# Kernel tuning notes

Measured on AMD Instinct MI355X. Metric: run time of the kernel, lower is better.

Reference implementation:

```python
import jax, jax.numpy as jnp
import numpy as np

N_GRAPHS = 4
NODES_PER_GRAPH = 8192
N_NODES = N_GRAPHS * NODES_PER_GRAPH
N_EDGES = N_NODES * 16
IN_DIM = 3
HID = 128
K_OUT = 512
MAX_WAVELENGTH = 10000.0


def _glorot(k, shape):
    lim = (6.0 / (shape[0] + shape[1])) ** 0.5
    return jax.random.uniform(k, shape, jnp.float32, -lim, lim)


def setup_inputs() -> dict:
    key = jax.random.key(0)
    ks = jax.random.split(key, 12)
    z = lambda *s: jnp.zeros(s, jnp.float32)
    return {
        "x": jax.random.normal(ks[0], (N_NODES, IN_DIM), jnp.float32),
        "mesh_pos": jax.random.uniform(ks[1], (N_NODES, 2), jnp.float32),
        "mesh_edges": jax.random.randint(ks[2], (N_EDGES, 2), 0, N_NODES, jnp.int32),
        "batch_idx": jnp.arange(N_NODES, dtype=jnp.int32) // NODES_PER_GRAPH,
        "proj_w": _glorot(ks[3], (IN_DIM, HID)), "proj_b": z(HID),
        "msg_w1": _glorot(ks[4], (2 * HID, HID)), "msg_b1": z(HID),
        "msg_w2": _glorot(ks[5], (HID, HID)), "msg_b2": z(HID),
        "upd_w1": _glorot(ks[6], (2 * HID, HID)), "upd_b1": z(HID),
        "upd_w2": _glorot(ks[7], (HID, HID)), "upd_b2": z(HID),
        "pool_rel_w": _glorot(ks[8], (HID, 1)), "pool_rel_b": z(1),
        "pool_root_w": _glorot(ks[9], (HID, 1)),
    }


def _sincos_embed(pos):
    # ContinuousSincosEmbed: HID=128, ndim=2 -> 64 channels per coord dim, 32 freqs
    dim_per_ndim = HID // 2
    omega = 1.0 / MAX_WAVELENGTH ** (jnp.arange(0, dim_per_ndim, 2, dtype=jnp.float32) / dim_per_ndim)
    ang = pos[:, :, None] * omega  # [N, ndim, 32]
    emb = jnp.concatenate([jnp.sin(ang), jnp.cos(ang)], axis=-1)  # [N, ndim, 64]
    return emb.reshape(pos.shape[0], HID)


def reference(x, mesh_pos, mesh_edges, batch_idx, proj_w, proj_b,
              msg_w1, msg_b1, msg_w2, msg_b2, upd_w1, upd_b1, upd_w2, upd_b2,
              pool_rel_w, pool_rel_b, pool_root_w):
    src, dst = mesh_edges[:, 0], mesh_edges[:, 1]  # edge_index[0]=j(src), [1]=i(dst)
    h = x @ proj_w + proj_b + _sincos_embed(mesh_pos)
    cnt = jnp.maximum(jax.ops.segment_sum(jnp.ones((N_EDGES,), h.dtype), dst, num_segments=N_NODES), 1.0)
    # message passing layer (depth=1): message MLP on [x_i, x_j], scatter-mean, residual update MLP
    m_in = jnp.concatenate([h[dst], h[src]], axis=-1)  # [E, 2H]
    m = jax.nn.silu(m_in @ msg_w1 + msg_b1) @ msg_w2 + msg_b2
    agg = jax.ops.segment_sum(m, dst, num_segments=N_NODES) / cnt[:, None]
    h = h + (jax.nn.silu(jnp.concatenate([h, agg], axis=-1) @ upd_w1 + upd_b1) @ upd_w2 + upd_b2)
    # SAGPooling score: GraphConv(HID,1,aggr='mean'), tanh nonlinearity
    nagg = jax.ops.segment_sum(h[src], dst, num_segments=N_NODES) / cnt[:, None]
    score = jnp.tanh((nagg @ pool_rel_w + pool_rel_b + h @ pool_root_w)[:, 0])
    # fixed top-k per graph (batch_idx is contiguous blocks of NODES_PER_GRAPH)
    topv, topi = jax.lax.top_k(score.reshape(N_GRAPHS, NODES_PER_GRAPH), K_OUT)
    perm = (topi + jnp.arange(N_GRAPHS, dtype=topi.dtype)[:, None] * NODES_PER_GRAPH).reshape(-1)
    x_pool = h[perm] * topv.reshape(-1)[:, None]
    batch_pool = jnp.repeat(jnp.arange(N_GRAPHS, dtype=batch_idx.dtype), K_OUT)
    return x_pool, batch_pool
```

## Files before the change

### kernel.cpp

```cpp
#include <hip/hip_runtime.h>
#include <hip/hip_bf16.h>
#include <math.h>

#define N_NODESC 32768
#define N_EDGESC 524288
#define NPG 8192
#define KOUT 512

typedef unsigned short u16;
typedef unsigned int u32;
typedef unsigned long long u64;

__device__ __forceinline__ float siluf(float x) {
    return x / (1.f + __expf(-x));
}

__global__ __launch_bounds__(256) void k_h0(const float* __restrict__ x,
                                            const float* __restrict__ pos,
                                            const float* __restrict__ pw,
                                            const float* __restrict__ pb,
                                            float* __restrict__ h,
                                            int* __restrict__ deg) {
    int gid = blockIdx.x * 256 + threadIdx.x;
    if (gid < N_NODESC) deg[gid] = 0;
    int node = blockIdx.x * 2 + (threadIdx.x >> 7);
    int c = threadIdx.x & 127;
    float x0 = x[node * 3 + 0];
    float x1 = x[node * 3 + 1];
    float x2 = x[node * 3 + 2];
    float acc = x0 * pw[c] + x1 * pw[128 + c] + x2 * pw[256 + c];
    acc += pb[c];
    int dim = c >> 6;
    int inner = c & 63;
    int jj = inner & 31;
    float p = pos[node * 2 + dim];
    float omega = exp2f(-(float)jj * 0.41524101186092027f);
    float ang = p * omega;
    acc += (inner < 32) ? __sinf(ang) : __cosf(ang);
    h[(size_t)node * 128 + c] = acc;
}

__global__ __launch_bounds__(256) void k_deg(const int* __restrict__ edges, int* __restrict__ deg) {
    int e = blockIdx.x * 256 + threadIdx.x;
    if (e < N_EDGESC) {
        int2 e2 = ((const int2*)edges)[e];
        atomicAdd(&deg[e2.y], 1);
    }
}

__global__ __launch_bounds__(1024) void k_scan(const int* __restrict__ deg,
                                               int* __restrict__ off, int* __restrict__ cur,
                                               float* __restrict__ rs, float* __restrict__ bg) {
    __shared__ int ls[1024];
    int tid = threadIdx.x;
    int base = tid * 32;
    int v[32];
    int s = 0;
#pragma unroll
    for (int j = 0; j < 32; j++) { v[j] = deg[base + j]; s += v[j]; }
    ls[tid] = s;
    __syncthreads();
    for (int ofs = 1; ofs < 1024; ofs <<= 1) {
        int t = (tid >= ofs) ? ls[tid - ofs] : 0;
        __syncthreads();
        ls[tid] += t;
        __syncthreads();
    }
    int run = ls[tid] - s;
#pragma unroll
    for (int j = 0; j < 32; j++) {
        off[base + j] = run;
        cur[base + j] = run;
        int d = v[j];
        rs[base + j] = 1.f / (float)(d > 0 ? d : 1);
        bg[base + j] = d > 0 ? 1.f : 0.f;
        run += d;
    }
}

__global__ __launch_bounds__(256) void k_fill(const int* __restrict__ edges,
                                              int* __restrict__ cur, int* __restrict__ csr) {
    int e = blockIdx.x * 256 + threadIdx.x;
    if (e < N_EDGESC) {
        int2 e2 = ((const int2*)edges)[e];
        int pos = atomicAdd(&cur[e2.y], 1);
        csr[pos] = e2.x;
    }
}

__global__ __launch_bounds__(256) void k_sortcsr(int* __restrict__ csr,
                                                 const int* __restrict__ off,
                                                 const int* __restrict__ deg) {
    int d = blockIdx.x * 4 + (threadIdx.x >> 6);
    int lane = threadIdx.x & 63;
    int o = off[d], n = deg[d];
    if (n <= 1) return;
    if (n <= 64) {
        int key = (lane < n) ? csr[o + lane] : 0x7FFFFFFF;
        for (int k = 2; k <= 64; k <<= 1) {
            for (int j = k >> 1; j > 0; j >>= 1) {
                int partner = __shfl_xor(key, j);
                bool asc = ((lane & k) == 0);
                bool keepMin = (((lane & j) == 0) == asc);
                key = keepMin ? min(key, partner) : max(key, partner);
            }
        }
        if (lane < n) csr[o + lane] = key;
    } else {
        if (lane == 0) {
            for (int i = o + 1; i < o + n; i++) {
                int x = csr[i];
                int j = i - 1;
                while (j >= o && csr[j] > x) { csr[j + 1] = csr[j]; j--; }
                csr[j + 1] = x;
            }
        }
    }
}

__global__ __launch_bounds__(256, 2) void gemm_dualw(const float* __restrict__ A,
                                                     const float* __restrict__ Wv,
                                                     const float* __restrict__ Wu,
                                                     const float* __restrict__ bu,
                                                     float* __restrict__ V, float* __restrict__ U) {
    __shared__ float Wsv[2][16 * 128];
    __shared__ float Wsu[2][16 * 128];
    int tid = threadIdx.x;
    int cg = tid & 31;
    int rg = tid >> 5;
    int m0 = blockIdx.x * 32 + rg * 4;
    int c0 = cg * 4;
    const float* Ar = A + (size_t)m0 * 128;

    float accv[4][4], accu[4][4];
#pragma unroll
    for (int r = 0; r < 4; r++)
#pragma unroll
        for (int c = 0; c < 4; c++) { accv[r][c] = 0.f; accu[r][c] = 0.f; }

#define STAGE_DW(buf, kc)                                                          \
    {                                                                              \
        const float4* Wgv = (const float4*)(Wv + (size_t)(kc) * 128);              \
        const float4* Wgu = (const float4*)(Wu + (size_t)(kc) * 128);              \
        float4* Wlv = (float4*)Wsv[buf];                                           \
        float4* Wlu = (float4*)Wsu[buf];                                           \
        _Pragma("unroll") for (int i = 0; i < 2; i++) {                            \
            Wlv[tid + i * 256] = Wgv[tid + i * 256];                               \
            Wlu[tid + i * 256] = Wgu[tid + i * 256];                               \
        }                                                                          \
    }

    STAGE_DW(0, 0)
    __syncthreads();
    for (int c = 0; c < 8; c++) {
        int buf = c & 1;
        if (c + 1 < 8) STAGE_DW(buf ^ 1, (c + 1) * 16)
        int kc = c * 16;
#pragma unroll
        for (int k0 = 0; k0 < 16; k0 += 4) {
            float4 a[4];
#pragma unroll
            for (int r = 0; r < 4; r++) a[r] = *(const float4*)(Ar + r * 128 + kc + k0);
#pragma unroll
            for (int kk = 0; kk < 4; kk++) {
                float4 wv = *(const float4*)(Wsv[buf] + (k0 + kk) * 128 + c0);
                float4 wu = *(const float4*)(Wsu[buf] + (k0 + kk) * 128 + c0);
#pragma unroll
                for (int r = 0; r < 4; r++) {
                    float aa = ((const float*)&a[r])[kk];
                    accv[r][0] += aa * wv.x; accv[r][1] += aa * wv.y;
                    accv[r][2] += aa * wv.z; accv[r][3] += aa * wv.w;
                    accu[r][0] += aa * wu.x; accu[r][1] += aa * wu.y;
                    accu[r][2] += aa * wu.z; accu[r][3] += aa * wu.w;
                }
            }
        }
        __syncthreads();
    }
#undef STAGE_DW
#pragma unroll
    for (int r = 0; r < 4; r++) {
        int row = m0 + r;
        float4 ov, ou;
        ov.x = accv[r][0]; ov.y = accv[r][1]; ov.z = accv[r][2]; ov.w = accv[r][3];
        ou.x = accu[r][0] + bu[c0];
        ou.y = accu[r][1] + bu[c0 + 1];
        ou.z = accu[r][2] + bu[c0 + 2];
        ou.w = accu[r][3] + bu[c0 + 3];
        *(float4*)(V + (size_t)row * 128 + c0) = ov;
        *(float4*)(U + (size_t)row * 128 + c0) = ou;
    }
}

__global__ __launch_bounds__(256, 2) void gemm_chain(const float* __restrict__ S,
                                                     float* __restrict__ h,
                                                     const float* __restrict__ W2,
                                                     const float* __restrict__ b2,
                                                     const float* __restrict__ rs,
                                                     const float* __restrict__ bg,
                                                     const float* __restrict__ U1a,
                                                     const float* __restrict__ U1b,
                                                     const float* __restrict__ ub1,
                                                     const float* __restrict__ U2,
                                                     const float* __restrict__ ub2,
                                                     const float* __restrict__ wrel,
                                                     const float* __restrict__ wroot,
                                                     float* __restrict__ pout,
                                                     float* __restrict__ rout) {
    __shared__ float Wc[2][32 * 128];
    __shared__ float T[32 * 128];
    int tid = threadIdx.x;
    int cg = tid & 31;
    int rg = tid >> 5;
    int m0 = blockIdx.x * 32 + rg * 4;
    int c0 = cg * 4;
    const float* Sr = S + (size_t)m0 * 128;
    const float* hr = h + (size_t)m0 * 128;

    float acc1[4][4], acc2[4][4];

#define ZERO(acc)                                                          \
    {                                                                      \
        _Pragma("unroll") for (int r = 0; r < 4; r++)                      \
            _Pragma("unroll") for (int c = 0; c < 4; c++) acc[r][c] = 0.f; \
    }
#define STAGE_W(buf, Wsrc, kc)                                             \
    {                                                                      \
        const float4* Wg = (const float4*)((Wsrc) + (size_t)(kc) * 128);   \
        float4* Wl = (float4*)Wc[buf];                                     \
        _Pragma("unroll") for (int i = 0; i < 4; i++)                      \
            Wl[tid + i * 256] = Wg[tid + i * 256];                         \
    }
#define COMPUTE_G(acc, buf, Abase, kc)                                     \
    {                                                                      \
        _Pragma("unroll") for (int k0 = 0; k0 < 32; k0 += 4) {             \
            float4 a[4];                                                   \
            _Pragma("unroll") for (int r = 0; r < 4; r++)                  \
                a[r] = *(const float4*)((Abase) + r * 128 + (kc) + k0);    \
            _Pragma("unroll") for (int kk = 0; kk < 4; kk++) {             \
                float4 wv = *(const float4*)(Wc[buf] + (k0 + kk) * 128 + c0); \
                _Pragma("unroll") for (int r = 0; r < 4; r++) {            \
                    float aa = ((const float*)&a[r])[kk];                  \
                    acc[r][0] += aa * wv.x; acc[r][1] += aa * wv.y;        \
                    acc[r][2] += aa * wv.z; acc[r][3] += aa * wv.w;        \
                }                                                          \
            }                                                              \
        }                                                                  \
    }
#define COMPUTE_T(acc, buf, kc)                                            \
    {                                                                      \
        _Pragma("unroll") for (int k0 = 0; k0 < 32; k0 += 4) {             \
            float4 a[4];                                                   \
            _Pragma("unroll") for (int r = 0; r < 4; r++)                  \
                a[r] = *(const float4*)(T + (rg * 4 + r) * 128 + (kc) + k0); \
            _Pragma("unroll") for (int kk = 0; kk < 4; kk++) {             \
                float4 wv = *(const float4*)(Wc[buf] + (k0 + kk) * 128 + c0); \
                _Pragma("unroll") for (int r = 0; r < 4; r++) {            \
                    float aa = ((const float*)&a[r])[kk];                  \
                    acc[r][0] += aa * wv.x; acc[r][1] += aa * wv.y;        \
                    acc[r][2] += aa * wv.z; acc[r][3] += aa * wv.w;        \
                }                                                          \
            }                                                              \
        }                                                                  \
    }
#define PASS_G(acc, Wsrc, Abase)                                           \
    {                                                                      \
        STAGE_W(0, Wsrc, 0)                                                \
        __syncthreads();                                                   \
        _Pragma("unroll") for (int c = 0; c < 4; c++) {                    \
            int buf = c & 1;                                               \
            if (c + 1 < 4) STAGE_W(buf ^ 1, Wsrc, (c + 1) * 32)            \
            COMPUTE_G(acc, buf, Abase, c * 32)                             \
            __syncthreads();                                               \
        }                                                                  \
    }
#define PASS_T(acc, Wsrc)                                                  \
    {                                                                      \
        STAGE_W(0, Wsrc, 0)                                                \
        __syncthreads();                                                   \
        _Pragma("unroll") for (int c = 0; c < 4; c++) {                    \
            int buf = c & 1;                                               \
            if (c + 1 < 4) STAGE_W(buf ^ 1, Wsrc, (c + 1) * 32)            \
            COMPUTE_T(acc, buf, c * 32)                                    \
            __syncthreads();                                               \
        }                                                                  \
    }

    ZERO(acc1)
    PASS_G(acc1, W2, Sr)
#pragma unroll
    for (int r = 0; r < 4; r++) {
        int row = m0 + r;
        float rsv = rs[row];
        float bgv = bg[row];
        float4 o;
        float* op = (float*)&o;
#pragma unroll
        for (int c = 0; c < 4; c++) {
            float xv = acc1[r][c];
            xv *= rsv;
            xv += b2[c0 + c] * bgv;
            op[c] = xv;
        }
        *(float4*)(T + (rg * 4 + r) * 128 + c0) = o;
    }
    __syncthreads();

    ZERO(acc1)
    PASS_G(acc1, U1a, hr)
    ZERO(acc2)
    PASS_T(acc2, U1b)
    __syncthreads();
#pragma unroll
    for (int r = 0; r < 4; r++) {
        float4 o;
        float* op = (float*)&o;
#pragma unroll
        for (int c = 0; c < 4; c++) {
            float xv = acc1[r][c];
            xv += acc2[r][c];
            xv += ub1[c0 + c];
            op[c] = siluf(xv);
        }
        *(float4*)(T + (rg * 4 + r) * 128 + c0) = o;
    }
    __syncthreads();

    ZERO(acc1)
    PASS_T(acc1, U2)
    float prel[4], prot[4];
#pragma unroll
    for (int r = 0; r < 4; r++) {
        int row = m0 + r;
        float4 o;
        float* op = (float*)&o;
#pragma unroll
        for (int c = 0; c < 4; c++) {
            float xv = acc1[r][c];
            xv *= 1.f;
            xv += ub2[c0 + c] * 1.f;
            xv += hr[r * 128 + c0 + c];
            op[c] = xv;
        }
        prel[r] = op[0] * wrel[c0] + op[1] * wrel[c0 + 1] + op[2] * wrel[c0 + 2] + op[3] * wrel[c0 + 3];
        prot[r] = op[0] * wroot[c0] + op[1] * wroot[c0 + 1] + op[2] * wroot[c0 + 2] + op[3] * wroot[c0 + 3];
        *(float4*)(h + (size_t)row * 128 + c0) = o;
    }
#pragma unroll
    for (int r = 0; r < 4; r++) {
        float a = prel[r], b = prot[r];
#pragma unroll
        for (int m = 1; m < 32; m <<= 1) {
            a += __shfl_xor(a, m);
            b += __shfl_xor(b, m);
        }
        if (cg == 0) { pout[m0 + r] = a; rout[m0 + r] = b; }
    }
#undef ZERO
#undef STAGE_W
#undef COMPUTE_G
#undef COMPUTE_T
#undef PASS_G
#undef PASS_T
}

__global__ __launch_bounds__(256) void k_accum_S(const float* __restrict__ v,
                                                 const int* __restrict__ csr, const int* __restrict__ off,
                                                 const int* __restrict__ deg, float* S) {
    int d = blockIdx.x * 4 + (threadIdx.x >> 6);
    int lane = threadIdx.x & 63;
    float* srow = S + (size_t)d * 128;
    float u0 = srow[lane];
    float u1 = srow[64 + lane];
    float a0 = 0.f, a1 = 0.f;
    int o = off[d], n = deg[d];
    for (int base = 0; base < n; base += 64) {
        int cnt = min(64, n - base);
        int sall = (lane < cnt) ? csr[o + base + lane] : 0;
        int j = 0;
        for (; j + 8 <= cnt; j += 8) {
            int s0 = __shfl(sall, j + 0), s1 = __shfl(sall, j + 1);
            int s2 = __shfl(sall, j + 2), s3 = __shfl(sall, j + 3);
            int s4 = __shfl(sall, j + 4), s5 = __shfl(sall, j + 5);
            int s6 = __shfl(sall, j + 6), s7 = __shfl(sall, j + 7);
            float v00 = v[(size_t)s0 * 128 + lane], v01 = v[(size_t)s0 * 128 + 64 + lane];
            float v10 = v[(size_t)s1 * 128 + lane], v11 = v[(size_t)s1 * 128 + 64 + lane];
            float v20 = v[(size_t)s2 * 128 + lane], v21 = v[(size_t)s2 * 128 + 64 + lane];
            float v30 = v[(size_t)s3 * 128 + lane], v31 = v[(size_t)s3 * 128 + 64 + lane];
            float v40 = v[(size_t)s4 * 128 + lane], v41 = v[(size_t)s4 * 128 + 64 + lane];
            float v50 = v[(size_t)s5 * 128 + lane], v51 = v[(size_t)s5 * 128 + 64 + lane];
            float v60 = v[(size_t)s6 * 128 + lane], v61 = v[(size_t)s6 * 128 + 64 + lane];
            float v70 = v[(size_t)s7 * 128 + lane], v71 = v[(size_t)s7 * 128 + 64 + lane];
            a0 += siluf(u0 + v00); a1 += siluf(u1 + v01);
            a0 += siluf(u0 + v10); a1 += siluf(u1 + v11);
            a0 += siluf(u0 + v20); a1 += siluf(u1 + v21);
            a0 += siluf(u0 + v30); a1 += siluf(u1 + v31);
            a0 += siluf(u0 + v40); a1 += siluf(u1 + v41);
            a0 += siluf(u0 + v50); a1 += siluf(u1 + v51);
            a0 += siluf(u0 + v60); a1 += siluf(u1 + v61);
            a0 += siluf(u0 + v70); a1 += siluf(u1 + v71);
        }
        for (; j < cnt; j++) {
            int s = __shfl(sall, j);
            a0 += siluf(u0 + v[(size_t)s * 128 + lane]);
            a1 += siluf(u1 + v[(size_t)s * 128 + 64 + lane]);
        }
    }
    srow[lane] = a0;
    srow[64 + lane] = a1;
}

__global__ __launch_bounds__(256) void k_score(const float* __restrict__ p, const float* __restrict__ r,
                                               const int* __restrict__ csr, const int* __restrict__ off,
                                               const int* __restrict__ deg, const float* __restrict__ relb,
                                               float* __restrict__ score) {
    int d = blockIdx.x * 4 + (threadIdx.x >> 6);
    int lane = threadIdx.x & 63;
    int o = off[d], n = deg[d];
    float a = 0.f;
    for (int j = lane; j < n; j += 64) a += p[csr[o + j]];
    for (int m = 32; m > 0; m >>= 1) a += __shfl_xor(a, m);
    if (lane == 0) {
        float cnt = (float)(n > 0 ? n : 1);
        score[d] = tanhf(a / cnt + relb[0] + r[d]);
    }
}

__global__ __launch_bounds__(1024) void k_topk(const float* __restrict__ score, const float* __restrict__ h,
                                               float* __restrict__ out) {
    __shared__ u32 ms[NPG];
    __shared__ u32 hist[256];
    __shared__ u32 sbuf[1024];
    __shared__ u64 sel[KOUT];
    __shared__ float ordv[KOUT];
    __shared__ int ordi[KOUT];
    __shared__ u32 selCnt, sPrefix, sNeed, sB;

    int g = blockIdx.x;
    int tid = threadIdx.x;

    for (int i = tid; i < NPG; i += 1024) {
        u32 u = __float_as_uint(score[(size_t)g * NPG + i]);
        ms[i] = (u & 0x80000000u) ? ~u : (u | 0x80000000u);
    }
    if (tid == 0) { sNeed = KOUT; sPrefix = 0; selCnt = 0; }
    __syncthreads();

    for (int pass = 0; pass < 4; pass++) {
        int shift = 24 - pass * 8;
        if (tid < 256) hist[tid] = 0;
        __syncthreads();
        u32 pfx = sPrefix;
        for (int i = tid; i < NPG; i += 1024) {
            u32 v = ms[i];
            if (pass == 0 || (v >> (shift + 8)) == pfx)
                atomicAdd(&hist[(v >> shift) & 255u], 1u);
        }
        __syncthreads();
        if (tid < 256) sbuf[tid] = hist[tid];
        __syncthreads();
        for (int ofs = 1; ofs < 256; ofs <<= 1) {
            u32 t = 0;
            if (tid < 256 && tid + ofs < 256) t = sbuf[tid + ofs];
            __syncthreads();
            if (tid < 256) sbuf[tid] += t;
            __syncthreads();
        }
        u32 need = sNeed;
        if (tid < 256) {
            if (sbuf[tid] >= need && (tid == 255 || sbuf[tid + 1] < need)) sB = (u32)tid;
        }
        __syncthreads();
        if (tid == 0) {
            u32 B = sB;
            u32 above = (B == 255) ? 0u : sbuf[B + 1];
            sNeed = need - above;
            sPrefix = (sPrefix << 8) | B;
        }
        __syncthreads();
    }
    u32 T = sPrefix;
    u32 rTie = sNeed;

    int base = tid * 8;
    u32 lc = 0;
#pragma unroll
    for (int j = 0; j < 8; j++) lc += (ms[base + j] == T);
    __syncthreads();
    sbuf[tid] = lc;
    __syncthreads();
    u32 own = lc;
    for (int ofs = 1; ofs < 1024; ofs <<= 1) {
        u32 t = (tid >= ofs) ? sbuf[tid - ofs] : 0;
        __syncthreads();
        sbuf[tid] += t;
        __syncthreads();
    }
    u32 excl = sbuf[tid] - own;

#pragma unroll
    for (int j = 0; j < 8; j++) {
        int i = base + j;
        u32 v = ms[i];
        bool pick = (v > T) || ((v == T) && (excl < rTie));
        if (v == T) excl++;
        if (pick) {
            u32 slot = atomicAdd(&selCnt, 1u);
            sel[slot] = ((u64)v << 32) | (u32)(NPG - 1 - i);
        }
    }
    __syncthreads();

    if (tid < KOUT) {
        u64 mine = sel[tid];
        int rank = 0;
        for (int j = 0; j < KOUT; j++) rank += (sel[j] > mine);
        u32 v = (u32)(mine >> 32);
        int idx = NPG - 1 - (int)(mine & 0xFFFFFFFFu);
        u32 uu = (v & 0x80000000u) ? (v & 0x7FFFFFFFu) : ~v;
        ordv[rank] = __uint_as_float(uu);
        ordi[rank] = idx;
    }
    __syncthreads();

    for (int t = tid; t < KOUT * 128; t += 1024) {
        int r = t >> 7, c = t & 127;
        int node = g * NPG + ordi[r];
        out[((size_t)g * KOUT + r) * 128 + c] = h[(size_t)node * 128 + c] * ordv[r];
    }
    for (int t = tid; t < KOUT; t += 1024)
        out[(size_t)4 * KOUT * 128 + (size_t)g * KOUT + t] = (float)g;
}

extern "C" void kernel_launch(void* const* d_in, const int* in_sizes, int n_in,
                              void* d_out, int out_size, void* d_ws, size_t ws_size,
                              hipStream_t stream) {
    const float* x        = (const float*)d_in[0];
    const float* mesh_pos = (const float*)d_in[1];
    const int*   edges    = (const int*)d_in[2];
    const float* proj_w   = (const float*)d_in[4];
    const float* proj_b   = (const float*)d_in[5];
    const float* msg_w1   = (const float*)d_in[6];
    const float* msg_b1   = (const float*)d_in[7];
    const float* msg_w2   = (const float*)d_in[8];
    const float* msg_b2   = (const float*)d_in[9];
    const float* upd_w1   = (const float*)d_in[10];
    const float* upd_b1   = (const float*)d_in[11];
    const float* upd_w2   = (const float*)d_in[12];
    const float* upd_b2   = (const float*)d_in[13];
    const float* pool_rel_w  = (const float*)d_in[14];
    const float* pool_rel_b  = (const float*)d_in[15];
    const float* pool_root_w = (const float*)d_in[16];
    float* out = (float*)d_out;

    char* w = (char*)d_ws;
    float* h  = (float*)(w);
    float* v  = (float*)(w + (1ull << 24));
    float* S  = (float*)(w + (2ull << 24));
    char* sm  = w + (3ull << 24);
    int*   deg   = (int*)(sm);
    int*   off   = (int*)(sm + 131072);
    int*   cur   = (int*)(sm + 262144);
    float* rsA   = (float*)(sm + 393216);
    float* bgA   = (float*)(sm + 524288);
    float* pp    = (float*)(sm + 655360);
    float* rr    = (float*)(sm + 786432);
    float* score = (float*)(sm + 917504);
    int*   csr   = (int*)(sm + 1048576);

    k_h0<<<N_NODESC / 2, 256, 0, stream>>>(x, mesh_pos, proj_w, proj_b, h, deg);
    k_deg<<<N_EDGESC / 256, 256, 0, stream>>>(edges, deg);
    k_scan<<<1, 1024, 0, stream>>>(deg, off, cur, rsA, bgA);
    k_fill<<<N_EDGESC / 256, 256, 0, stream>>>(edges, cur, csr);
    k_sortcsr<<<N_NODESC / 4, 256, 0, stream>>>(csr, off, deg);

    gemm_dualw<<<1024, 256, 0, stream>>>(h, msg_w1 + 128 * 128, msg_w1, msg_b1, v, S);
    k_accum_S<<<N_NODESC / 4, 256, 0, stream>>>(v, csr, off, deg, S);
    gemm_chain<<<1024, 256, 0, stream>>>(S, h, msg_w2, msg_b2, rsA, bgA,
                                         upd_w1, upd_w1 + 128 * 128, upd_b1,
                                         upd_w2, upd_b2,
                                         pool_rel_w, pool_root_w, pp, rr);

    k_score<<<N_NODESC / 4, 256, 0, stream>>>(pp, rr, csr, off, deg, pool_rel_b, score);
    k_topk<<<4, 1024, 0, stream>>>(score, h, out);
}
```

Baseline: 374.6 us.

## Fuse CSR neighbor sort into accumulation kernel and shrink chain GEMM K-tile

Removes the separate k_sortcsr launch by sorting each node's neighbor list in registers (two keys per lane, up to 128 entries) inside k_accum_S, then feeding the sorted indices straight from registers into the gather loop. The gather now loads float2 per lane instead of two scalar loads. Separately, gemm_chain's weight staging tile shrinks from 32 to 16 rows with twice as many pipeline stages, lowering shared memory use. This saves a launch plus one global read and write pass over the CSR array, but adds sort work to the gather kernel and more barriers in the GEMM.

```diff
diff --git a/kernel.cpp b/kernel.cpp
--- a/kernel.cpp
+++ b/kernel.cpp
@@ -88,36 +88,6 @@
     }
 }
 
-__global__ __launch_bounds__(256) void k_sortcsr(int* __restrict__ csr,
-                                                 const int* __restrict__ off,
-                                                 const int* __restrict__ deg) {
-    int d = blockIdx.x * 4 + (threadIdx.x >> 6);
-    int lane = threadIdx.x & 63;
-    int o = off[d], n = deg[d];
-    if (n <= 1) return;
-    if (n <= 64) {
-        int key = (lane < n) ? csr[o + lane] : 0x7FFFFFFF;
-        for (int k = 2; k <= 64; k <<= 1) {
-            for (int j = k >> 1; j > 0; j >>= 1) {
-                int partner = __shfl_xor(key, j);
-                bool asc = ((lane & k) == 0);
-                bool keepMin = (((lane & j) == 0) == asc);
-                key = keepMin ? min(key, partner) : max(key, partner);
-            }
-        }
-        if (lane < n) csr[o + lane] = key;
-    } else {
-        if (lane == 0) {
-            for (int i = o + 1; i < o + n; i++) {
-                int x = csr[i];
-                int j = i - 1;
-                while (j >= o && csr[j] > x) { csr[j + 1] = csr[j]; j--; }
-                csr[j + 1] = x;
-            }
-        }
-    }
-}
-
 __global__ __launch_bounds__(256, 2) void gemm_dualw(const float* __restrict__ A,
                                                      const float* __restrict__ Wv,
                                                      const float* __restrict__ Wu,
@@ -207,7 +177,7 @@
                                                      const float* __restrict__ wroot,
                                                      float* __restrict__ pout,
                                                      float* __restrict__ rout) {
-    __shared__ float Wc[2][32 * 128];
+    __shared__ float Wc[2][16 * 128];
     __shared__ float T[32 * 128];
     int tid = threadIdx.x;
     int cg = tid & 31;
@@ -228,12 +198,12 @@
     {                                                                      \
         const float4* Wg = (const float4*)((Wsrc) + (size_t)(kc) * 128);   \
         float4* Wl = (float4*)Wc[buf];                                     \
-        _Pragma("unroll") for (int i = 0; i < 4; i++)                      \
-            Wl[tid + i * 256] = Wg[tid + i * 256];                         \
+        Wl[tid] = Wg[tid];                                                 \
+        Wl[tid + 256] = Wg[tid + 256];                                     \
     }
 #define COMPUTE_G(acc, buf, Abase, kc)                                     \
     {                                                                      \
-        _Pragma("unroll") for (int k0 = 0; k0 < 32; k0 += 4) {             \
+        _Pragma("unroll") for (int k0 = 0; k0 < 16; k0 += 4) {             \
             float4 a[4];                                                   \
             _Pragma("unroll") for (int r = 0; r < 4; r++)                  \
                 a[r] = *(const float4*)((Abase) + r * 128 + (kc) + k0);    \
@@ -249,7 +219,7 @@
     }
 #define COMPUTE_T(acc, buf, kc)                                            \
     {                                                                      \
-        _Pragma("unroll") for (int k0 = 0; k0 < 32; k0 += 4) {             \
+        _Pragma("unroll") for (int k0 = 0; k0 < 16; k0 += 4) {             \
             float4 a[4];                                                   \
             _Pragma("unroll") for (int r = 0; r < 4; r++)                  \
                 a[r] = *(const float4*)(T + (rg * 4 + r) * 128 + (kc) + k0); \
@@ -267,10 +237,10 @@
     {                                                                      \
         STAGE_W(0, Wsrc, 0)                                                \
         __syncthreads();                                                   \
-        _Pragma("unroll") for (int c = 0; c < 4; c++) {                    \
+        _Pragma("unroll") for (int c = 0; c < 8; c++) {                    \
             int buf = c & 1;                                               \
-            if (c + 1 < 4) STAGE_W(buf ^ 1, Wsrc, (c + 1) * 32)            \
-            COMPUTE_G(acc, buf, Abase, c * 32)                             \
+            if (c + 1 < 8) STAGE_W(buf ^ 1, Wsrc, (c + 1) * 16)            \
+            COMPUTE_G(acc, buf, Abase, c * 16)                             \
             __syncthreads();                                               \
         }                                                                  \
     }
@@ -278,10 +248,10 @@
     {                                                                      \
         STAGE_W(0, Wsrc, 0)                                                \
         __syncthreads();                                                   \
-        _Pragma("unroll") for (int c = 0; c < 4; c++) {                    \
+        _Pragma("unroll") for (int c = 0; c < 8; c++) {                    \
             int buf = c & 1;                                               \
-            if (c + 1 < 4) STAGE_W(buf ^ 1, Wsrc, (c + 1) * 32)            \
-            COMPUTE_T(acc, buf, c * 32)                                    \
+            if (c + 1 < 8) STAGE_W(buf ^ 1, Wsrc, (c + 1) * 16)            \
+            COMPUTE_T(acc, buf, c * 16)                                    \
             __syncthreads();                                               \
         }                                                                  \
     }
@@ -365,49 +335,99 @@
 }
 
 __global__ __launch_bounds__(256) void k_accum_S(const float* __restrict__ v,
-                                                 const int* __restrict__ csr, const int* __restrict__ off,
+                                                 int* __restrict__ csr, const int* __restrict__ off,
                                                  const int* __restrict__ deg, float* S) {
     int d = blockIdx.x * 4 + (threadIdx.x >> 6);
     int lane = threadIdx.x & 63;
+    int o = off[d], n = deg[d];
     float* srow = S + (size_t)d * 128;
-    float u0 = srow[lane];
-    float u1 = srow[64 + lane];
-    float a0 = 0.f, a1 = 0.f;
-    int o = off[d], n = deg[d];
+    float2 u = *(const float2*)(srow + lane * 2);
+    float2 a = {0.f, 0.f};
+
+    int key0 = 0x7FFFFFFF, key1 = 0x7FFFFFFF;
+    bool small = (n <= 128);
+    if (small) {
+        if (n > 1) {
+            int i0 = 2 * lane, i1 = 2 * lane + 1;
+            if (i0 < n) key0 = csr[o + i0];
+            if (i1 < n) key1 = csr[o + i1];
+            for (int k = 2; k <= 128; k <<= 1) {
+                for (int j = k >> 1; j >= 2; j >>= 1) {
+                    int p0 = __shfl_xor(key0, j >> 1);
+                    int p1 = __shfl_xor(key1, j >> 1);
+                    int vi0 = 2 * lane, vi1 = vi0 + 1;
+                    bool keep0 = (((vi0 & j) == 0) == ((vi0 & k) == 0));
+                    bool keep1 = (((vi1 & j) == 0) == ((vi1 & k) == 0));
+                    key0 = keep0 ? min(key0, p0) : max(key0, p0);
+                    key1 = keep1 ? min(key1, p1) : max(key1, p1);
+                }
+                {
+                    bool asc = (((2 * lane) & k) == 0);
+                    int lo = min(key0, key1), hi = max(key0, key1);
+                    key0 = asc ? lo : hi;
+                    key1 = asc ? hi : lo;
+                }
+            }
+            if (2 * lane < n) csr[o + 2 * lane] = key0;
+            if (2 * lane + 1 < n) csr[o + 2 * lane + 1] = key1;
+        } else if (n == 1) {
+            key0 = csr[o];
+            key0 = __shfl(key0, 0);
+        }
+    } else {
+        if (lane == 0) {
+            for (int i = o + 1; i < o + n; i++) {
+                int x = csr[i];
+                int j = i - 1;
+                while (j >= o && csr[j] > x) { csr[j + 1] = csr[j]; j--; }
+                csr[j + 1] = x;
+            }
+        }
+        __threadfence();
+    }
+
     for (int base = 0; base < n; base += 64) {
         int cnt = min(64, n - base);
-        int sall = (lane < cnt) ? csr[o + base + lane] : 0;
+        int sall;
+        if (small) {
+            int src = (base + lane) >> 1;
+            int e0 = __shfl(key0, src);
+            int e1 = __shfl(key1, src);
+            sall = (lane & 1) ? e1 : e0;
+        } else {
+            sall = (lane < cnt) ? csr[o + base + lane] : 0;
+        }
         int j = 0;
         for (; j + 8 <= cnt; j += 8) {
             int s0 = __shfl(sall, j + 0), s1 = __shfl(sall, j + 1);
             int s2 = __shfl(sall, j + 2), s3 = __shfl(sall, j + 3);
             int s4 = __shfl(sall, j + 4), s5 = __shfl(sall, j + 5);
             int s6 = __shfl(sall, j + 6), s7 = __shfl(sall, j + 7);
-            float v00 = v[(size_t)s0 * 128 + lane], v01 = v[(size_t)s0 * 128 + 64 + lane];
-            float v10 = v[(size_t)s1 * 128 + lane], v11 = v[(size_t)s1 * 128 + 64 + lane];
-            float v20 = v[(size_t)s2 * 128 + lane], v21 = v[(size_t)s2 * 128 + 64 + lane];
-            float v30 = v[(size_t)s3 * 128 + lane], v31 = v[(size_t)s3 * 128 + 64 + lane];
-            float v40 = v[(size_t)s4 * 128 + lane], v41 = v[(size_t)s4 * 128 + 64 + lane];
-            float v50 = v[(size_t)s5 * 128 + lane], v51 = v[(size_t)s5 * 128 + 64 + lane];
-            float v60 = v[(size_t)s6 * 128 + lane], v61 = v[(size_t)s6 * 128 + 64 + lane];
-            float v70 = v[(size_t)s7 * 128 + lane], v71 = v[(size_t)s7 * 128 + 64 + lane];
-            a0 += siluf(u0 + v00); a1 += siluf(u1 + v01);
-            a0 += siluf(u0 + v10); a1 += siluf(u1 + v11);
-            a0 += siluf(u0 + v20); a1 += siluf(u1 + v21);
-            a0 += siluf(u0 + v30); a1 += siluf(u1 + v31);
-            a0 += siluf(u0 + v40); a1 += siluf(u1 + v41);
-            a0 += siluf(u0 + v50); a1 += siluf(u1 + v51);
-            a0 += siluf(u0 + v60); a1 += siluf(u1 + v61);
-            a0 += siluf(u0 + v70); a1 += siluf(u1 + v71);
+            float2 w0 = *(const float2*)(v + (size_t)s0 * 128 + lane * 2);
+            float2 w1 = *(const float2*)(v + (size_t)s1 * 128 + lane * 2);
+            float2 w2 = *(const float2*)(v + (size_t)s2 * 128 + lane * 2);
+            float2 w3 = *(const float2*)(v + (size_t)s3 * 128 + lane * 2);
+            float2 w4 = *(const float2*)(v + (size_t)s4 * 128 + lane * 2);
+            float2 w5 = *(const float2*)(v + (size_t)s5 * 128 + lane * 2);
+            float2 w6 = *(const float2*)(v + (size_t)s6 * 128 + lane * 2);
+            float2 w7 = *(const float2*)(v + (size_t)s7 * 128 + lane * 2);
+            a.x += siluf(u.x + w0.x); a.y += siluf(u.y + w0.y);
+            a.x += siluf(u.x + w1.x); a.y += siluf(u.y + w1.y);
+            a.x += siluf(u.x + w2.x); a.y += siluf(u.y + w2.y);
+            a.x += siluf(u.x + w3.x); a.y += siluf(u.y + w3.y);
+            a.x += siluf(u.x + w4.x); a.y += siluf(u.y + w4.y);
+            a.x += siluf(u.x + w5.x); a.y += siluf(u.y + w5.y);
+            a.x += siluf(u.x + w6.x); a.y += siluf(u.y + w6.y);
+            a.x += siluf(u.x + w7.x); a.y += siluf(u.y + w7.y);
         }
         for (; j < cnt; j++) {
             int s = __shfl(sall, j);
-            a0 += siluf(u0 + v[(size_t)s * 128 + lane]);
-            a1 += siluf(u1 + v[(size_t)s * 128 + 64 + lane]);
-        }
-    }
-    srow[lane] = a0;
-    srow[64 + lane] = a1;
+            float2 w = *(const float2*)(v + (size_t)s * 128 + lane * 2);
+            a.x += siluf(u.x + w.x);
+            a.y += siluf(u.y + w.y);
+        }
+    }
+    *(float2*)(srow + lane * 2) = a;
 }
 
 __global__ __launch_bounds__(256) void k_score(const float* __restrict__ p, const float* __restrict__ r,
@@ -572,7 +592,6 @@
     k_deg<<<N_EDGESC / 256, 256, 0, stream>>>(edges, deg);
     k_scan<<<1, 1024, 0, stream>>>(deg, off, cur, rsA, bgA);
     k_fill<<<N_EDGESC / 256, 256, 0, stream>>>(edges, cur, csr);
-    k_sortcsr<<<N_NODESC / 4, 256, 0, stream>>>(csr, off, deg);
 
     gemm_dualw<<<1024, 256, 0, stream>>>(h, msg_w1 + 128 * 128, msg_w1, msg_b1, v, S);
     k_accum_S<<<N_NODESC / 4, 256, 0, stream>>>(v, csr, off, deg, S);
```

New measurement: 400.1 us. 6.8% more time.
